# Kernel optimization log

Hardware: AMD Instinct MI355X
Metric: run time of the kernel (lower is better)

Reference implementation:

```python
import jax, jax.numpy as jnp
import numpy as np

B, N, C, H = 8, 1024, 768, 12
D = C // H
SCALE = D ** -0.5


def setup_inputs() -> dict:
    key = jax.random.key(0)
    ks = jax.random.split(key, 6)
    std = 0.02
    return {
        "x": jax.random.normal(ks[0], (B, N, C), dtype=jnp.float32),
        "w_qkv": jax.random.normal(ks[1], (3 * C, C), dtype=jnp.float32) * std,
        "w_proj": jax.random.normal(ks[2], (C, C), dtype=jnp.float32) * std,
        "b_proj": jnp.zeros((C,), dtype=jnp.float32),
        "conv_l_w": jax.random.normal(ks[3], (H, H), dtype=jnp.float32) * std,
        "conv_w_w": jax.random.normal(ks[4], (H, H), dtype=jnp.float32) * std,
    }


def reference(x, w_qkv, w_proj, b_proj, conv_l_w, conv_w_w):
    Bx, Nx, Cx = x.shape
    # qkv projection: torch Linear uses x @ W^T
    qkv = (x @ w_qkv.T).reshape(Bx, Nx, 3, H, D)
    qkv = jnp.transpose(qkv, (2, 0, 3, 1, 4))  # [3, B, H, N, D]
    q, k, v = qkv[0], qkv[1], qkv[2]
    q = q * SCALE
    attn = jnp.einsum("bhnd,bhmd->bhnm", q, k)  # [B,H,N,N]
    # 1x1 conv across heads (conv_l)
    attn = jnp.einsum("oh,bhnm->bonm", conv_l_w, attn)
    attn = jax.nn.softmax(attn, axis=-1)
    # 1x1 conv across heads (conv_w)
    attn = jnp.einsum("oh,bhnm->bonm", conv_w_w, attn)
    out = jnp.einsum("bhnm,bhmd->bhnd", attn, v)
    out = jnp.transpose(out, (0, 2, 1, 3)).reshape(Bx, Nx, Cx)
    return out @ w_proj.T + b_proj
```

## Files before the change

### kernel.cpp

```cpp
#include <hip/hip_runtime.h>
#include <hip/hip_bf16.h>

typedef __attribute__((ext_vector_type(8))) short short8;
typedef __attribute__((ext_vector_type(4))) short short4v;
typedef __attribute__((ext_vector_type(4))) float float4v;

#define NB 8
#define NH 12
#define NN 1024
#define ND 64
#define NC 768

__device__ __forceinline__ short f2bf(float f) {
  __hip_bfloat16 h = __float2bfloat16(f);
  union { __hip_bfloat16 h; short s; } u; u.h = h; return u.s;
}
__device__ __forceinline__ unsigned pk2(float a, float b) {
  unsigned ua = (unsigned short)f2bf(a);
  unsigned ub = (unsigned short)f2bf(b);
  return ua | (ub << 16);
}

template<int MODE>
__global__ __launch_bounds__(256, 2)
void gemm_kernel(const void* __restrict__ Ap, const float* __restrict__ Bw,
                 const float* __restrict__ bias,
                 __hip_bfloat16* __restrict__ Qo, __hip_bfloat16* __restrict__ Ko,
                 __hip_bfloat16* __restrict__ VTo, float* __restrict__ Out)
{
  __shared__ short As[128 * 40];
  __shared__ short Bs[128 * 40];
  const int tid = threadIdx.x;
  const int w = tid >> 6, lane = tid & 63, lr = lane & 15, lg = lane >> 4;
  const int wr = w >> 1, wc = w & 1;
  const int n0 = blockIdx.x * 128, m0 = blockIdx.y * 128;

  float4v acc[4][4];
  #pragma unroll
  for (int i = 0; i < 4; i++)
    #pragma unroll
    for (int j = 0; j < 4; j++)
      acc[i][j] = (float4v){0.f, 0.f, 0.f, 0.f};

  for (int kt = 0; kt < 768; kt += 32) {
    if (MODE == 0) {
      const float* A = (const float*)Ap;
      #pragma unroll
      for (int i2 = 0; i2 < 4; i2++) {
        int c = tid + 256 * i2;
        int row = c >> 3, c4 = c & 7;
        float4v v = *(const float4v*)(A + (size_t)(m0 + row) * 768 + kt + c4 * 4);
        short4v s = { f2bf(v[0]), f2bf(v[1]), f2bf(v[2]), f2bf(v[3]) };
        *(short4v*)(&As[row * 40 + c4 * 4]) = s;
      }
    } else {
      const __hip_bfloat16* A = (const __hip_bfloat16*)Ap;
      #pragma unroll
      for (int i2 = 0; i2 < 2; i2++) {
        int c = tid + 256 * i2;
        int row = c >> 2, c8 = c & 3;
        *(short8*)(&As[row * 40 + c8 * 8]) =
            *(const short8*)(A + (size_t)(m0 + row) * 768 + kt + c8 * 8);
      }
    }
    #pragma unroll
    for (int i2 = 0; i2 < 4; i2++) {
      int c = tid + 256 * i2;
      int row = c >> 3, c4 = c & 7;
      float4v v = *(const float4v*)(Bw + (size_t)(n0 + row) * 768 + kt + c4 * 4);
      short4v s = { f2bf(v[0]), f2bf(v[1]), f2bf(v[2]), f2bf(v[3]) };
      *(short4v*)(&Bs[row * 40 + c4 * 4]) = s;
    }
    __syncthreads();

    short8 af[4], bfr[4];
    #pragma unroll
    for (int i = 0; i < 4; i++)
      af[i] = *(const short8*)(&As[(wr * 64 + i * 16 + lr) * 40 + lg * 8]);
    #pragma unroll
    for (int j = 0; j < 4; j++)
      bfr[j] = *(const short8*)(&Bs[(wc * 64 + j * 16 + lr) * 40 + lg * 8]);
    #pragma unroll
    for (int i = 0; i < 4; i++)
      #pragma unroll
      for (int j = 0; j < 4; j++)
        acc[i][j] = __builtin_amdgcn_mfma_f32_16x16x32_bf16(af[i], bfr[j], acc[i][j], 0, 0, 0);
    __syncthreads();
  }

  #pragma unroll
  for (int i = 0; i < 4; i++) {
    #pragma unroll
    for (int j = 0; j < 4; j++) {
      #pragma unroll
      for (int r = 0; r < 4; r++) {
        float val = acc[i][j][r];
        int mg_ = m0 + wr * 64 + i * 16 + lg * 4 + r;
        int ng_ = n0 + wc * 64 + j * 16 + lr;
        if (MODE == 0) {
          int s = ng_ / 768;
          int rem = ng_ - s * 768;
          int h = rem >> 6, d = rem & 63;
          int b = mg_ >> 10, n = mg_ & 1023;
          if (s == 0)
            Qo[(((size_t)b * NH + h) * NN + n) * ND + d] = __float2bfloat16(val * 0.125f);
          else if (s == 1)
            Ko[(((size_t)b * NH + h) * NN + n) * ND + d] = __float2bfloat16(val);
          else
            VTo[(((size_t)b * NH + h) * ND + d) * NN + n] = __float2bfloat16(val);
        } else {
          Out[(size_t)mg_ * NC + ng_] = val + bias[ng_];
        }
      }
    }
  }
}

__global__ __launch_bounds__(256, 2)
void attn_kernel(const __hip_bfloat16* __restrict__ Qg, const __hip_bfloat16* __restrict__ Kg,
                 const __hip_bfloat16* __restrict__ VTg,
                 const float* __restrict__ convl, const float* __restrict__ convw,
                 __hip_bfloat16* __restrict__ AOut)
{
  __shared__ short Sb[32 * 576];
  __shared__ short pm[16 * 648];
  __shared__ short lwA[512];
  __shared__ short wwT[512];

  const int tid = threadIdx.x;
  const int w = tid >> 6, lane = tid & 63, lr = lane & 15, lg = lane >> 4;
  const int b = blockIdx.x >> 6;
  const int n0 = (blockIdx.x & 63) * 16;
  const float4v zf = (float4v){0.f, 0.f, 0.f, 0.f};

  for (int i = tid; i < 512; i += 256) {
    int r = i >> 5, k = i & 31;
    bool v = (r < 12) && (k < 12);
    lwA[i] = v ? f2bf(convl[r * 12 + k]) : (short)0;
    wwT[i] = v ? f2bf(convw[r * 12 + k]) : (short)0;
  }
  for (int i = tid; i < 512; i += 256) {
    short* p = &Sb[i * 36 + 12];
    #pragma unroll
    for (int j = 0; j < 24; j++) p[j] = 0;
  }

  short8 qf[3][2];
  #pragma unroll
  for (int hh = 0; hh < 3; hh++)
    #pragma unroll
    for (int ks = 0; ks < 2; ks++)
      qf[hh][ks] = *(const short8*)(Qg +
          (((size_t)b * NH + w * 3 + hh) * NN + n0 + lr) * ND + ks * 32 + lg * 8);
  __syncthreads();
  const short8 lwf = *(const short8*)(&lwA[lr * 32 + lg * 8]);
  const short8 wwf = *(const short8*)(&wwT[lr * 32 + lg * 8]);

  float Lacc[4][4];
  #pragma unroll
  for (int r = 0; r < 4; r++)
    #pragma unroll
    for (int nn = 0; nn < 4; nn++) Lacc[r][nn] = 0.f;

  for (int t = 0; t < 32; t++) {
    const int m0t = t * 32;
    #pragma unroll
    for (int hh = 0; hh < 3; hh++) {
      const int h = w * 3 + hh;
      const size_t kbase = (((size_t)b * NH + h) * NN + m0t) * ND;
      #pragma unroll
      for (int j = 0; j < 2; j++) {
        float4v a = zf;
        #pragma unroll
        for (int ks = 0; ks < 2; ks++) {
          short8 kb = *(const short8*)(Kg + kbase + (size_t)(j * 16 + lr) * ND + ks * 32 + lg * 8);
          a = __builtin_amdgcn_mfma_f32_16x16x32_bf16(qf[hh][ks], kb, a, 0, 0, 0);
        }
        #pragma unroll
        for (int r = 0; r < 4; r++)
          Sb[((lg * 4 + r) * 2 + j) * 576 + lr * 36 + h] = f2bf(a[r]);
      }
    }
    __syncthreads();
    #pragma unroll
    for (int cc = 0; cc < 8; cc++) {
      const int c = w * 8 + cc;
      short8 sb = *(const short8*)(&Sb[c * 576 + lr * 36 + lg * 8]);
      float4v d = __builtin_amdgcn_mfma_f32_16x16x32_bf16(lwf, sb, zf, 0, 0, 0);
      #pragma unroll
      for (int r = 0; r < 4; r++)
        Lacc[r][cc >> 1] += __expf(d[r]);
    }
    __syncthreads();
  }
  float logLreg[4][4];
  #pragma unroll
  for (int r = 0; r < 4; r++)
    #pragma unroll
    for (int nn = 0; nn < 4; nn++) {
      float v = Lacc[r][nn];
      v += __shfl_xor(v, 1);
      v += __shfl_xor(v, 2);
      v += __shfl_xor(v, 4);
      v += __shfl_xor(v, 8);
      logLreg[r][nn] = __logf(v);
    }

  float4v oacc[3][4];
  #pragma unroll
  for (int hh = 0; hh < 3; hh++)
    #pragma unroll
    for (int jd = 0; jd < 4; jd++) oacc[hh][jd] = zf;

  for (int t = 0; t < 32; t++) {
    const int m0t = t * 32;
    #pragma unroll
    for (int hh = 0; hh < 3; hh++) {
      const int h = w * 3 + hh;
      const size_t kbase = (((size_t)b * NH + h) * NN + m0t) * ND;
      #pragma unroll
      for (int j = 0; j < 2; j++) {
        float4v a = zf;
        #pragma unroll
        for (int ks = 0; ks < 2; ks++) {
          short8 kb = *(const short8*)(Kg + kbase + (size_t)(j * 16 + lr) * ND + ks * 32 + lg * 8);
          a = __builtin_amdgcn_mfma_f32_16x16x32_bf16(qf[hh][ks], kb, a, 0, 0, 0);
        }
        #pragma unroll
        for (int r = 0; r < 4; r++)
          Sb[((lg * 4 + r) * 2 + j) * 576 + lr * 36 + h] = f2bf(a[r]);
      }
    }
    __syncthreads();
    #pragma unroll
    for (int cc = 0; cc < 8; cc++) {
      const int c = w * 8 + cc;
      short8 sb = *(const short8*)(&Sb[c * 576 + lr * 36 + lg * 8]);
      float4v d = __builtin_amdgcn_mfma_f32_16x16x32_bf16(lwf, sb, zf, 0, 0, 0);
      float p0 = __expf(d[0] - logLreg[0][cc >> 1]);
      float p1 = __expf(d[1] - logLreg[1][cc >> 1]);
      float p2 = __expf(d[2] - logLreg[2][cc >> 1]);
      float p3 = __expf(d[3] - logLreg[3][cc >> 1]);
      unsigned* dst = (unsigned*)(&Sb[c * 576 + lr * 36 + lg * 4]);
      dst[0] = pk2(p0, p1);
      dst[1] = pk2(p2, p3);
    }
    asm volatile("s_waitcnt lgkmcnt(0)" ::: "memory");
    __builtin_amdgcn_sched_barrier(0);
    #pragma unroll
    for (int cc = 0; cc < 8; cc++) {
      const int c = w * 8 + cc;
      short8 pb = *(const short8*)(&Sb[c * 576 + lr * 36 + lg * 8]);
      float4v d = __builtin_amdgcn_mfma_f32_16x16x32_bf16(pb, wwf, zf, 0, 0, 0);
      unsigned* dst = (unsigned*)(&pm[lr * 648 + (c >> 1) * 40 + (c & 1) * 16 + lg * 4]);
      dst[0] = pk2(d[0], d[1]);
      dst[1] = pk2(d[2], d[3]);
    }
    __syncthreads();
    #pragma unroll
    for (int hh = 0; hh < 3; hh++) {
      const int o2 = w * 3 + hh;
      short8 pf = *(const short8*)(&pm[o2 * 648 + lr * 40 + lg * 8]);
      const size_t vbase = ((size_t)b * NH + o2) * ND * NN;
      #pragma unroll
      for (int jd = 0; jd < 4; jd++) {
        short8 vt = *(const short8*)(VTg + vbase + (size_t)(jd * 16 + lr) * NN + m0t + lg * 8);
        oacc[hh][jd] = __builtin_amdgcn_mfma_f32_16x16x32_bf16(vt, pf, oacc[hh][jd], 0, 0, 0);
      }
    }
    __syncthreads();
  }

  #pragma unroll
  for (int hh = 0; hh < 3; hh++) {
    const int o2 = w * 3 + hh;
    #pragma unroll
    for (int jd = 0; jd < 4; jd++) {
      size_t base = ((size_t)b * NN + n0 + lr) * NC + o2 * 64 + jd * 16 + lg * 4;
      unsigned* dst = (unsigned*)(&AOut[base]);
      dst[0] = pk2(oacc[hh][jd][0], oacc[hh][jd][1]);
      dst[1] = pk2(oacc[hh][jd][2], oacc[hh][jd][3]);
    }
  }
}

extern "C" void kernel_launch(void* const* d_in, const int* in_sizes, int n_in,
                              void* d_out, int out_size, void* d_ws, size_t ws_size,
                              hipStream_t stream) {
  const float* x      = (const float*)d_in[0];
  const float* w_qkv  = (const float*)d_in[1];
  const float* w_proj = (const float*)d_in[2];
  const float* b_proj = (const float*)d_in[3];
  const float* conv_l = (const float*)d_in[4];
  const float* conv_w = (const float*)d_in[5];
  float* out = (float*)d_out;

  const size_t NE = (size_t)NB * NH * NN * ND;
  __hip_bfloat16* Qb = (__hip_bfloat16*)d_ws;
  __hip_bfloat16* Kb = Qb + NE;
  __hip_bfloat16* VT = Kb + NE;
  __hip_bfloat16* AO = VT + NE;

  gemm_kernel<0><<<dim3(18, 64), 256, 0, stream>>>(x, w_qkv, nullptr, Qb, Kb, VT, nullptr);
  attn_kernel<<<dim3(512), 256, 0, stream>>>(Qb, Kb, VT, conv_l, conv_w, AO);
  gemm_kernel<1><<<dim3(6, 64), 256, 0, stream>>>(AO, w_proj, b_proj, nullptr, nullptr, nullptr, out);
}
```

Baseline: 386.5 us.

## Software-pipeline K prefetch and skew PV step across attention loop iterations

K tiles are prefetched into registers one iteration ahead in both passes, so global load latency overlaps the QK MFMAs and LDS work. The second pass is skewed so the P·V accumulation for tile t-1 runs alongside the score computation for tile t, with V loads issued early. The block-to-(batch, row) mapping is also changed so consecutive blocks cover different batches. These changes raise register pressure (kreg, vt0, vt1), which under launch_bounds(256,2) may cause spills.

```diff
diff --git a/kernel.cpp b/kernel.cpp
--- a/kernel.cpp
+++ b/kernel.cpp
@@ -129,8 +129,8 @@
 
   const int tid = threadIdx.x;
   const int w = tid >> 6, lane = tid & 63, lr = lane & 15, lg = lane >> 4;
-  const int b = blockIdx.x >> 6;
-  const int n0 = (blockIdx.x & 63) * 16;
+  const int b = blockIdx.x & 7;
+  const int n0 = (blockIdx.x >> 3) * 16;
   const float4v zf = (float4v){0.f, 0.f, 0.f, 0.f};
 
   for (int i = tid; i < 512; i += 256) {
@@ -152,6 +152,22 @@
     for (int ks = 0; ks < 2; ks++)
       qf[hh][ks] = *(const short8*)(Qg +
           (((size_t)b * NH + w * 3 + hh) * NN + n0 + lr) * ND + ks * 32 + lg * 8);
+
+  short8 kreg[3][2][2];
+  auto loadK = [&](int t) {
+    const int m0t = t * 32;
+    #pragma unroll
+    for (int hh = 0; hh < 3; hh++) {
+      const size_t kbase = (((size_t)b * NH + w * 3 + hh) * NN + m0t) * ND;
+      #pragma unroll
+      for (int j = 0; j < 2; j++)
+        #pragma unroll
+        for (int ks = 0; ks < 2; ks++)
+          kreg[hh][j][ks] = *(const short8*)(Kg + kbase +
+              (size_t)(j * 16 + lr) * ND + ks * 32 + lg * 8);
+    }
+  };
+  loadK(0);
   __syncthreads();
   const short8 lwf = *(const short8*)(&lwA[lr * 32 + lg * 8]);
   const short8 wwf = *(const short8*)(&wwT[lr * 32 + lg * 8]);
@@ -163,24 +179,21 @@
     for (int nn = 0; nn < 4; nn++) Lacc[r][nn] = 0.f;
 
   for (int t = 0; t < 32; t++) {
-    const int m0t = t * 32;
     #pragma unroll
     for (int hh = 0; hh < 3; hh++) {
       const int h = w * 3 + hh;
-      const size_t kbase = (((size_t)b * NH + h) * NN + m0t) * ND;
       #pragma unroll
       for (int j = 0; j < 2; j++) {
         float4v a = zf;
         #pragma unroll
-        for (int ks = 0; ks < 2; ks++) {
-          short8 kb = *(const short8*)(Kg + kbase + (size_t)(j * 16 + lr) * ND + ks * 32 + lg * 8);
-          a = __builtin_amdgcn_mfma_f32_16x16x32_bf16(qf[hh][ks], kb, a, 0, 0, 0);
-        }
+        for (int ks = 0; ks < 2; ks++)
+          a = __builtin_amdgcn_mfma_f32_16x16x32_bf16(qf[hh][ks], kreg[hh][j][ks], a, 0, 0, 0);
         #pragma unroll
         for (int r = 0; r < 4; r++)
           Sb[((lg * 4 + r) * 2 + j) * 576 + lr * 36 + h] = f2bf(a[r]);
       }
     }
+    loadK(t < 31 ? t + 1 : 0);
     __syncthreads();
     #pragma unroll
     for (int cc = 0; cc < 8; cc++) {
@@ -212,60 +225,87 @@
     #pragma unroll
     for (int jd = 0; jd < 4; jd++) oacc[hh][jd] = zf;
 
-  for (int t = 0; t < 32; t++) {
-    const int m0t = t * 32;
-    #pragma unroll
-    for (int hh = 0; hh < 3; hh++) {
-      const int h = w * 3 + hh;
-      const size_t kbase = (((size_t)b * NH + h) * NN + m0t) * ND;
-      #pragma unroll
-      for (int j = 0; j < 2; j++) {
-        float4v a = zf;
-        #pragma unroll
-        for (int ks = 0; ks < 2; ks++) {
-          short8 kb = *(const short8*)(Kg + kbase + (size_t)(j * 16 + lr) * ND + ks * 32 + lg * 8);
-          a = __builtin_amdgcn_mfma_f32_16x16x32_bf16(qf[hh][ks], kb, a, 0, 0, 0);
+  for (int t = 0; t <= 32; t++) {
+    short8 vt0[3][2];
+    if (t > 0) {
+      const int m0v = (t - 1) * 32;
+      #pragma unroll
+      for (int hh = 0; hh < 3; hh++) {
+        const size_t vbase = ((size_t)b * NH + w * 3 + hh) * ND * NN;
+        #pragma unroll
+        for (int jj = 0; jj < 2; jj++)
+          vt0[hh][jj] = *(const short8*)(VTg + vbase +
+              (size_t)(jj * 16 + lr) * NN + m0v + lg * 8);
+      }
+    }
+    if (t < 32) {
+      #pragma unroll
+      for (int hh = 0; hh < 3; hh++) {
+        const int h = w * 3 + hh;
+        #pragma unroll
+        for (int j = 0; j < 2; j++) {
+          float4v a = zf;
+          #pragma unroll
+          for (int ks = 0; ks < 2; ks++)
+            a = __builtin_amdgcn_mfma_f32_16x16x32_bf16(qf[hh][ks], kreg[hh][j][ks], a, 0, 0, 0);
+          #pragma unroll
+          for (int r = 0; r < 4; r++)
+            Sb[((lg * 4 + r) * 2 + j) * 576 + lr * 36 + h] = f2bf(a[r]);
         }
-        #pragma unroll
-        for (int r = 0; r < 4; r++)
-          Sb[((lg * 4 + r) * 2 + j) * 576 + lr * 36 + h] = f2bf(a[r]);
-      }
-    }
-    __syncthreads();
-    #pragma unroll
-    for (int cc = 0; cc < 8; cc++) {
-      const int c = w * 8 + cc;
-      short8 sb = *(const short8*)(&Sb[c * 576 + lr * 36 + lg * 8]);
-      float4v d = __builtin_amdgcn_mfma_f32_16x16x32_bf16(lwf, sb, zf, 0, 0, 0);
-      float p0 = __expf(d[0] - logLreg[0][cc >> 1]);
-      float p1 = __expf(d[1] - logLreg[1][cc >> 1]);
-      float p2 = __expf(d[2] - logLreg[2][cc >> 1]);
-      float p3 = __expf(d[3] - logLreg[3][cc >> 1]);
-      unsigned* dst = (unsigned*)(&Sb[c * 576 + lr * 36 + lg * 4]);
-      dst[0] = pk2(p0, p1);
-      dst[1] = pk2(p2, p3);
-    }
-    asm volatile("s_waitcnt lgkmcnt(0)" ::: "memory");
-    __builtin_amdgcn_sched_barrier(0);
-    #pragma unroll
-    for (int cc = 0; cc < 8; cc++) {
-      const int c = w * 8 + cc;
-      short8 pb = *(const short8*)(&Sb[c * 576 + lr * 36 + lg * 8]);
-      float4v d = __builtin_amdgcn_mfma_f32_16x16x32_bf16(pb, wwf, zf, 0, 0, 0);
-      unsigned* dst = (unsigned*)(&pm[lr * 648 + (c >> 1) * 40 + (c & 1) * 16 + lg * 4]);
-      dst[0] = pk2(d[0], d[1]);
-      dst[1] = pk2(d[2], d[3]);
-    }
-    __syncthreads();
-    #pragma unroll
-    for (int hh = 0; hh < 3; hh++) {
-      const int o2 = w * 3 + hh;
-      short8 pf = *(const short8*)(&pm[o2 * 648 + lr * 40 + lg * 8]);
-      const size_t vbase = ((size_t)b * NH + o2) * ND * NN;
-      #pragma unroll
-      for (int jd = 0; jd < 4; jd++) {
-        short8 vt = *(const short8*)(VTg + vbase + (size_t)(jd * 16 + lr) * NN + m0t + lg * 8);
-        oacc[hh][jd] = __builtin_amdgcn_mfma_f32_16x16x32_bf16(vt, pf, oacc[hh][jd], 0, 0, 0);
+      }
+      if (t < 31) loadK(t + 1);
+    }
+    if (t > 0) {
+      const int m0v = (t - 1) * 32;
+      short8 pf[3];
+      #pragma unroll
+      for (int hh = 0; hh < 3; hh++)
+        pf[hh] = *(const short8*)(&pm[(w * 3 + hh) * 648 + lr * 40 + lg * 8]);
+      #pragma unroll
+      for (int hh = 0; hh < 3; hh++)
+        #pragma unroll
+        for (int jj = 0; jj < 2; jj++)
+          oacc[hh][jj] = __builtin_amdgcn_mfma_f32_16x16x32_bf16(vt0[hh][jj], pf[hh], oacc[hh][jj], 0, 0, 0);
+      short8 vt1[3][2];
+      #pragma unroll
+      for (int hh = 0; hh < 3; hh++) {
+        const size_t vbase = ((size_t)b * NH + w * 3 + hh) * ND * NN;
+        #pragma unroll
+        for (int jj = 0; jj < 2; jj++)
+          vt1[hh][jj] = *(const short8*)(VTg + vbase +
+              (size_t)((2 + jj) * 16 + lr) * NN + m0v + lg * 8);
+      }
+      #pragma unroll
+      for (int hh = 0; hh < 3; hh++)
+        #pragma unroll
+        for (int jj = 0; jj < 2; jj++)
+          oacc[hh][2 + jj] = __builtin_amdgcn_mfma_f32_16x16x32_bf16(vt1[hh][jj], pf[hh], oacc[hh][2 + jj], 0, 0, 0);
+    }
+    __syncthreads();
+    if (t < 32) {
+      #pragma unroll
+      for (int cc = 0; cc < 8; cc++) {
+        const int c = w * 8 + cc;
+        short8 sb = *(const short8*)(&Sb[c * 576 + lr * 36 + lg * 8]);
+        float4v d = __builtin_amdgcn_mfma_f32_16x16x32_bf16(lwf, sb, zf, 0, 0, 0);
+        float p0 = __expf(d[0] - logLreg[0][cc >> 1]);
+        float p1 = __expf(d[1] - logLreg[1][cc >> 1]);
+        float p2 = __expf(d[2] - logLreg[2][cc >> 1]);
+        float p3 = __expf(d[3] - logLreg[3][cc >> 1]);
+        unsigned* dst = (unsigned*)(&Sb[c * 576 + lr * 36 + lg * 4]);
+        dst[0] = pk2(p0, p1);
+        dst[1] = pk2(p2, p3);
+      }
+      asm volatile("s_waitcnt lgkmcnt(0)" ::: "memory");
+      __builtin_amdgcn_sched_barrier(0);
+      #pragma unroll
+      for (int cc = 0; cc < 8; cc++) {
+        const int c = w * 8 + cc;
+        short8 pb = *(const short8*)(&Sb[c * 576 + lr * 36 + lg * 8]);
+        float4v d = __builtin_amdgcn_mfma_f32_16x16x32_bf16(pb, wwf, zf, 0, 0, 0);
+        unsigned* dst = (unsigned*)(&pm[lr * 648 + (c >> 1) * 40 + (c & 1) * 16 + lg * 4]);
+        dst[0] = pk2(d[0], d[1]);
+        dst[1] = pk2(d[2], d[3]);
       }
     }
     __syncthreads();
```

New measurement: 392.0 us. About the same (+1.4%).
